# Performance work log

Measured on AMD Instinct MI355X. Metric: run time of the kernel, lower is better.

The kernel has to match this reference:

```python
import jax, jax.numpy as jnp
import numpy as np

B, T, D = 2, 2048, 2048
H, HD = 16, 128
I = 5632
CAP = 0.5
EPS = 1e-6
NEG = -1e9


def _rmsnorm(x, w):
    v = x.astype(jnp.float32)
    v = v * jax.lax.rsqrt(jnp.mean(v * v, axis=-1, keepdims=True) + EPS)
    return v.astype(x.dtype) * w


def _rotate_half(x):
    x1, x2 = jnp.split(x, 2, axis=-1)
    return jnp.concatenate([-x2, x1], axis=-1)


def setup_inputs() -> dict:
    key = jax.random.key(0)
    ks = jax.random.split(key, 20)
    s = 0.02
    inp = {
        'hidden_states': jax.random.normal(ks[0], (B, T, D), jnp.float32),
        'original': jax.random.normal(ks[1], (B, T, D), jnp.float32),
        'posterior': jax.random.normal(ks[2], (B, T, D), jnp.float32),
        'prior': jax.random.normal(ks[3], (B, T, D), jnp.float32),
        'cos': jax.random.normal(ks[4], (B, T, HD), jnp.float32),
        'sin': jax.random.normal(ks[5], (B, T, HD), jnp.float32),
        'position_ids': jax.random.randint(ks[6], (B, T), 0, T),
        'q_w': jax.random.normal(ks[7], (D, H * HD), jnp.float32) * s,
        'q_b': jnp.zeros((H * HD,), jnp.float32),
        'k_w': jax.random.normal(ks[8], (D, H * HD), jnp.float32) * s,
        'k_b': jnp.zeros((H * HD,), jnp.float32),
        'v_w': jax.random.normal(ks[9], (D, H * HD), jnp.float32) * s,
        'v_b': jnp.zeros((H * HD,), jnp.float32),
        'o_w': jax.random.normal(ks[10], (H * HD, D), jnp.float32) * s,
        'ln1_w': jnp.ones((D,), jnp.float32),
        'ln2_w': jnp.ones((D,), jnp.float32),
        'gate_w': jax.random.normal(ks[11], (D, I), jnp.float32) * s,
        'up_w': jax.random.normal(ks[12], (D, I), jnp.float32) * s,
        'down_w': jax.random.normal(ks[13], (I, D), jnp.float32) * s,
        'beta_ce': jnp.array(-0.5, jnp.float32),
        'beta_cu': jnp.array(-0.8, jnp.float32),
        'ce_off': jnp.array(1.0, jnp.float32),
    }
    return inp


def reference(hidden_states, original, posterior, prior, cos, sin, position_ids,
              q_w, q_b, k_w, k_b, v_w, v_b, o_w, ln1_w, ln2_w,
              gate_w, up_w, down_w, beta_ce, beta_cu, ce_off):
    Bt, Tt, Dt = hidden_states.shape
    K = int(CAP * Tt)  # tokens selected per batch row
    # --- router: surprise scores ---
    cu = jnp.linalg.norm(original - posterior, axis=-1)  # [B,T]
    ce = jnp.linalg.norm(posterior - prior, axis=-1)     # [B,T]
    scores = beta_cu * cu + beta_ce * (ce + ce_off)      # [B,T]
    # --- capacity top-k per batch row, keep temporal order ---
    _, topi = jax.lax.top_k(scores, K)                   # [B,K]
    token_idx2 = jnp.sort(topi, axis=-1)                 # [B,K]
    sel_scores = jnp.take_along_axis(scores, token_idx2, axis=1)  # [B,K]
    b_idx = jnp.repeat(jnp.arange(Bt), K)                # [S]
    t_idx = token_idx2.reshape(-1)                       # [S]
    S = Bt * K
    sel_h = hidden_states[b_idx, t_idx]                  # [S,D]
    cos_g = cos[b_idx, t_idx][None, None]                # [1,1,S,HD]
    sin_g = sin[b_idx, t_idx][None, None]
    # --- Qwen2 decoder block on the single gathered sequence [1,S,D] ---
    x = sel_h[None]
    h = _rmsnorm(x, ln1_w)
    q = (h @ q_w + q_b).reshape(1, S, H, HD).transpose(0, 2, 1, 3)  # [1,H,S,HD]
    k = (h @ k_w + k_b).reshape(1, S, H, HD).transpose(0, 2, 1, 3)
    v = (h @ v_w + v_b).reshape(1, S, H, HD).transpose(0, 2, 1, 3)
    q = q * cos_g + _rotate_half(q) * sin_g
    k = k * cos_g + _rotate_half(k) * sin_g
    att = jnp.einsum('bhqd,bhkd->bhqk', q, k) / np.sqrt(HD)
    causal = jnp.tril(jnp.ones((S, S), bool))
    att = jnp.where(causal, att, NEG)
    att = jax.nn.softmax(att.astype(jnp.float32), axis=-1).astype(x.dtype)
    o = jnp.einsum('bhqk,bhkd->bhqd', att, v)
    o = o.transpose(0, 2, 1, 3).reshape(1, S, H * HD) @ o_w
    x = x + o
    h = _rmsnorm(x, ln2_w)
    mlp = (jax.nn.silu(h @ gate_w) * (h @ up_w)) @ down_w
    x = x + mlp
    processed = x[0]                                     # [S,D]
    # --- gated update + scatter back ---
    gate = jax.nn.sigmoid(sel_scores.reshape(-1))[:, None]
    updated = sel_h + (processed - sel_h) * gate
    output = hidden_states.at[b_idx, t_idx].set(updated)
    return output
```

## Files before the change

### kernel.cpp

```cpp
#include <hip/hip_runtime.h>


typedef unsigned short u16;
typedef unsigned int u32;
typedef short bf16x8 __attribute__((ext_vector_type(8)));
typedef float f32x4 __attribute__((ext_vector_type(4)));

#define T_LEN 2048
#define D_DIM 2048
#define B_DIM 2
#define H_NUM 16
#define HD_DIM 128
#define I_DIM 5632
#define K_CAP 1024
#define S_TOT 2048
#define QKV_N 6144
#define GU_N 11264

__device__ __forceinline__ u16 f2bf(float f) {
  union { float f; u32 u; } a; a.f = f;
  u32 r = a.u + 0x7fffu + ((a.u >> 16) & 1u);
  return (u16)(r >> 16);
}
__device__ __forceinline__ float bf2f(u16 x) {
  return __uint_as_float((u32)x << 16);
}

__device__ __forceinline__ void gld_lds16(const void* g, void* l) {
  void* gg = const_cast<void*>(g);
  __builtin_amdgcn_global_load_lds(
      (__attribute__((address_space(1))) u32*)gg,
      (__attribute__((address_space(3))) u32*)l, 16, 0, 0);
}

__global__ __launch_bounds__(256)
void router_kernel(const float* __restrict__ orig, const float* __restrict__ post,
                   const float* __restrict__ prior, const float* __restrict__ bce,
                   const float* __restrict__ bcu, const float* __restrict__ coff,
                   float* __restrict__ scores) {
  const int row = blockIdx.x;
  const size_t base = (size_t)row * D_DIM;
  float s1 = 0.f, s2 = 0.f;
  for (int d = threadIdx.x * 4; d < D_DIM; d += 1024) {
    float4 o = *(const float4*)(orig + base + d);
    float4 p = *(const float4*)(post + base + d);
    float4 r = *(const float4*)(prior + base + d);
    float a;
    a = o.x - p.x; s1 += a * a;  a = o.y - p.y; s1 += a * a;
    a = o.z - p.z; s1 += a * a;  a = o.w - p.w; s1 += a * a;
    a = p.x - r.x; s2 += a * a;  a = p.y - r.y; s2 += a * a;
    a = p.z - r.z; s2 += a * a;  a = p.w - r.w; s2 += a * a;
  }
#pragma unroll
  for (int k = 32; k; k >>= 1) { s1 += __shfl_down(s1, k); s2 += __shfl_down(s2, k); }
  __shared__ float r1[4], r2[4];
  const int wv = threadIdx.x >> 6;
  if ((threadIdx.x & 63) == 0) { r1[wv] = s1; r2[wv] = s2; }
  __syncthreads();
  if (threadIdx.x == 0) {
    float cu = sqrtf(r1[0] + r1[1] + r1[2] + r1[3]);
    float ce = sqrtf(r2[0] + r2[1] + r2[2] + r2[3]);
    scores[row] = bcu[0] * cu + bce[0] * (ce + coff[0]);
  }
}

__global__ __launch_bounds__(256)
void rank_kernel(const float* __restrict__ scores, int* __restrict__ rnk) {
  const int b = blockIdx.y;
  const int t = blockIdx.x * 256 + threadIdx.x;
  __shared__ float s[T_LEN];
  for (int u = threadIdx.x; u < T_LEN; u += 256) s[u] = scores[b * T_LEN + u];
  __syncthreads();
  const float st = s[t];
  int r = 0;
  for (int u = 0; u < T_LEN; ++u) {
    float su = s[u];
    r += ((su > st) || (su == st && u < t)) ? 1 : 0;
  }
  rnk[b * T_LEN + t] = r;
}

__global__ __launch_bounds__(256)
void compact_kernel(const float* __restrict__ scores, const int* __restrict__ rnk,
                    int* __restrict__ tidx, float* __restrict__ gate) {
  const int b = blockIdx.x;
  const int base = b * T_LEN;
  __shared__ int csum[256];
  int f[8]; int loc = 0;
  const int t0 = threadIdx.x * 8;
#pragma unroll
  for (int i = 0; i < 8; ++i) { f[i] = (rnk[base + t0 + i] < K_CAP) ? 1 : 0; loc += f[i]; }
  csum[threadIdx.x] = loc;
  __syncthreads();
  if (threadIdx.x == 0) {
    int run = 0;
    for (int i = 0; i < 256; ++i) { int tmp = csum[i]; csum[i] = run; run += tmp; }
  }
  __syncthreads();
  int pos = csum[threadIdx.x];
#pragma unroll
  for (int i = 0; i < 8; ++i) {
    if (f[i]) {
      float sc = scores[base + t0 + i];
      tidx[b * K_CAP + pos] = t0 + i;
      gate[b * K_CAP + pos] = 1.f / (1.f + __expf(-sc));
      ++pos;
    }
  }
}

__global__ __launch_bounds__(256)
void transpose_bf16_kernel(const float* __restrict__ W, u16* __restrict__ Wt,
                           int K, int N) {
  __shared__ float tile[32][33];
  const int bn = blockIdx.x * 32, bk = blockIdx.y * 32;
  const int tx = threadIdx.x & 31, ty = threadIdx.x >> 5;
#pragma unroll
  for (int i = 0; i < 32; i += 8)
    tile[ty + i][tx] = W[(size_t)(bk + ty + i) * N + bn + tx];
  __syncthreads();
#pragma unroll
  for (int i = 0; i < 32; i += 8)
    Wt[(size_t)(bn + ty + i) * K + bk + tx] = f2bf(tile[tx][ty + i]);
}

__global__ __launch_bounds__(256)
void vtrans_kernel(const u16* __restrict__ qkv, u16* __restrict__ VT) {
  __shared__ u16 tile[32][34];
  const int s0 = blockIdx.x * 32;
  const int c0 = blockIdx.y * 32;
  const int tx = threadIdx.x & 31, ty = threadIdx.x >> 5;
#pragma unroll
  for (int i = 0; i < 32; i += 8)
    tile[ty + i][tx] = qkv[(size_t)(s0 + ty + i) * QKV_N + 4096 + c0 + tx];
  __syncthreads();
#pragma unroll
  for (int i = 0; i < 32; i += 8)
    VT[(size_t)(c0 + ty + i) * S_TOT + s0 + tx] = tile[tx][ty + i];
}

__global__ __launch_bounds__(256)
void rmsnorm_kernel(const float* __restrict__ X, const int* __restrict__ tidx,
                    const float* __restrict__ w, float* __restrict__ xcopy,
                    u16* __restrict__ Y) {
  const int s = blockIdx.x;
  const float* row;
  if (tidx) {
    const int b = s >> 10;
    const int t = tidx[s];
    row = X + ((size_t)b * T_LEN + t) * D_DIM;
  } else {
    row = X + (size_t)s * D_DIM;
  }
  const int d0 = threadIdx.x * 4;
  float4 v0 = *(const float4*)(row + d0);
  float4 v1 = *(const float4*)(row + d0 + 1024);
  float ss = v0.x*v0.x + v0.y*v0.y + v0.z*v0.z + v0.w*v0.w
           + v1.x*v1.x + v1.y*v1.y + v1.z*v1.z + v1.w*v1.w;
#pragma unroll
  for (int k = 32; k; k >>= 1) ss += __shfl_down(ss, k);
  __shared__ float red[4];
  if ((threadIdx.x & 63) == 0) red[threadIdx.x >> 6] = ss;
  __syncthreads();
  const float tot = red[0] + red[1] + red[2] + red[3];
  const float rms = rsqrtf(tot * (1.0f / D_DIM) + 1e-6f);
  if (xcopy) {
    *(float4*)(xcopy + (size_t)s * D_DIM + d0) = v0;
    *(float4*)(xcopy + (size_t)s * D_DIM + d0 + 1024) = v1;
  }
  const float4 w0 = *(const float4*)(w + d0);
  const float4 w1 = *(const float4*)(w + d0 + 1024);
  u16* yp = Y + (size_t)s * D_DIM;
  u32 a0 = (u32)f2bf(v0.x * rms * w0.x) | ((u32)f2bf(v0.y * rms * w0.y) << 16);
  u32 a1 = (u32)f2bf(v0.z * rms * w0.z) | ((u32)f2bf(v0.w * rms * w0.w) << 16);
  *(uint2*)(yp + d0) = make_uint2(a0, a1);
  u32 b0 = (u32)f2bf(v1.x * rms * w1.x) | ((u32)f2bf(v1.y * rms * w1.y) << 16);
  u32 b1 = (u32)f2bf(v1.z * rms * w1.z) | ((u32)f2bf(v1.w * rms * w1.w) << 16);
  *(uint2*)(yp + d0 + 1024) = make_uint2(b0, b1);
}

__global__ __launch_bounds__(256)
void gemm_bf16_kernel(const u16* __restrict__ A, const u16* __restrict__ Bt,
                      float* __restrict__ C, u16* __restrict__ Cbf,
                      const float* __restrict__ bias,
                      const float* __restrict__ resid, int N, int K) {
  __shared__ u16 As[128 * 32];
  __shared__ u16 Bs[128 * 32];
  const int tid = threadIdx.x;
  const int w = tid >> 6, l = tid & 63;
  const int row0 = blockIdx.y * 128, col0 = blockIdx.x * 128;
  const int wr = (w >> 1) * 64, wc = (w & 1) * 64;
  const int am = l & 15, ak = (l >> 4) * 8;
  const int srow = l >> 2, scol = (l & 3) * 8;

  f32x4 acc[4][4] = {};

  const u16* Abase = A + (size_t)(row0 + srow) * K + scol;
  const u16* Bbase = Bt + (size_t)(col0 + srow) * K + scol;
  const int R0 = (w * 2) * 16, R1 = (w * 2 + 1) * 16;

  for (int k0 = 0; k0 < K; k0 += 32) {
    gld_lds16(Abase + (size_t)R0 * K + k0, &As[R0 * 32]);
    gld_lds16(Abase + (size_t)R1 * K + k0, &As[R1 * 32]);
    gld_lds16(Bbase + (size_t)R0 * K + k0, &Bs[R0 * 32]);
    gld_lds16(Bbase + (size_t)R1 * K + k0, &Bs[R1 * 32]);
    __syncthreads();
    bf16x8 af[4], bfr[4];
#pragma unroll
    for (int i = 0; i < 4; ++i) af[i] = *(const bf16x8*)&As[(wr + i * 16 + am) * 32 + ak];
#pragma unroll
    for (int j = 0; j < 4; ++j) bfr[j] = *(const bf16x8*)&Bs[(wc + j * 16 + am) * 32 + ak];
#pragma unroll
    for (int i = 0; i < 4; ++i)
#pragma unroll
      for (int j = 0; j < 4; ++j)
        acc[i][j] = __builtin_amdgcn_mfma_f32_16x16x32_bf16(af[i], bfr[j], acc[i][j], 0, 0, 0);
    __syncthreads();
  }

  const int rb = wr + (l >> 4) * 4;
  const int cb = wc + (l & 15);
#pragma unroll
  for (int i = 0; i < 4; ++i) {
#pragma unroll
    for (int j = 0; j < 4; ++j) {
      const int colg = col0 + cb + j * 16;
      const float bv = bias ? bias[colg] : 0.0f;
#pragma unroll
      for (int r = 0; r < 4; ++r) {
        const int rowg = row0 + rb + i * 16 + r;
        const size_t idx = (size_t)rowg * N + colg;
        float v = acc[i][j][r] + bv;
        if (resid) v += resid[idx];
        if (Cbf) Cbf[idx] = f2bf(v);
        else C[idx] = v;
      }
    }
  }
}

__global__ __launch_bounds__(256)
void gemm_bf16_splitk_kernel(const u16* __restrict__ A, const u16* __restrict__ Bt,
                             float* __restrict__ P, int N, int K, int kLen) {
  __shared__ u16 As[128 * 32];
  __shared__ u16 Bs[128 * 32];
  const int tid = threadIdx.x;
  const int w = tid >> 6, l = tid & 63;
  const int row0 = blockIdx.y * 128, col0 = blockIdx.x * 128;
  const int kbeg = blockIdx.z * kLen, kend = kbeg + kLen;
  float* Pz = P + (size_t)blockIdx.z * S_TOT * N;
  const int wr = (w >> 1) * 64, wc = (w & 1) * 64;
  const int am = l & 15, ak = (l >> 4) * 8;
  const int srow = l >> 2, scol = (l & 3) * 8;

  f32x4 acc[4][4] = {};

  const u16* Abase = A + (size_t)(row0 + srow) * K + scol;
  const u16* Bbase = Bt + (size_t)(col0 + srow) * K + scol;
  const int R0 = (w * 2) * 16, R1 = (w * 2 + 1) * 16;

  for (int k0 = kbeg; k0 < kend; k0 += 32) {
    gld_lds16(Abase + (size_t)R0 * K + k0, &As[R0 * 32]);
    gld_lds16(Abase + (size_t)R1 * K + k0, &As[R1 * 32]);
    gld_lds16(Bbase + (size_t)R0 * K + k0, &Bs[R0 * 32]);
    gld_lds16(Bbase + (size_t)R1 * K + k0, &Bs[R1 * 32]);
    __syncthreads();
    bf16x8 af[4], bfr[4];
#pragma unroll
    for (int i = 0; i < 4; ++i) af[i] = *(const bf16x8*)&As[(wr + i * 16 + am) * 32 + ak];
#pragma unroll
    for (int j = 0; j < 4; ++j) bfr[j] = *(const bf16x8*)&Bs[(wc + j * 16 + am) * 32 + ak];
#pragma unroll
    for (int i = 0; i < 4; ++i)
#pragma unroll
      for (int j = 0; j < 4; ++j)
        acc[i][j] = __builtin_amdgcn_mfma_f32_16x16x32_bf16(af[i], bfr[j], acc[i][j], 0, 0, 0);
    __syncthreads();
  }

  const int rb = wr + (l >> 4) * 4;
  const int cb = wc + (l & 15);
#pragma unroll
  for (int i = 0; i < 4; ++i)
#pragma unroll
    for (int j = 0; j < 4; ++j) {
      const int colg = col0 + cb + j * 16;
#pragma unroll
      for (int r = 0; r < 4; ++r) {
        const int rowg = row0 + rb + i * 16 + r;
        Pz[(size_t)rowg * N + colg] = acc[i][j][r];
      }
    }
}

__global__ __launch_bounds__(256)
void add3_kernel(float* __restrict__ acc, const float* __restrict__ p1,
                 const float* __restrict__ resid) {
  const size_t i = ((size_t)blockIdx.x * 256 + threadIdx.x) * 4;
  float4 a = *(const float4*)(acc + i);
  float4 b = *(const float4*)(p1 + i);
  float4 c = *(const float4*)(resid + i);
  a.x += b.x + c.x; a.y += b.y + c.y; a.z += b.z + c.z; a.w += b.w + c.w;
  *(float4*)(acc + i) = a;
}

__global__ __launch_bounds__(256)
void down_finish_kernel(const float* __restrict__ P, const float* __restrict__ x1,
                        const int* __restrict__ tidx, const float* __restrict__ gate,
                        const float* __restrict__ hs, float* __restrict__ out) {
  const int s = blockIdx.x;
  const int b = s >> 10;
  const int t = tidx[s];
  const float gg = gate[s];
  const size_t src = (size_t)s * D_DIM;
  const size_t dst = ((size_t)b * T_LEN + t) * D_DIM;
  const size_t plane = (size_t)S_TOT * D_DIM;
  for (int d = threadIdx.x * 4; d < D_DIM; d += 1024) {
    float4 p0 = *(const float4*)(P + src + d);
    float4 p1 = *(const float4*)(P + plane + src + d);
    float4 xr = *(const float4*)(x1 + src + d);
    float4 hv = *(const float4*)(hs + dst + d);
    float4 r;
    r.x = hv.x + (p0.x + p1.x + xr.x - hv.x) * gg;
    r.y = hv.y + (p0.y + p1.y + xr.y - hv.y) * gg;
    r.z = hv.z + (p0.z + p1.z + xr.z - hv.z) * gg;
    r.w = hv.w + (p0.w + p1.w + xr.w - hv.w) * gg;
    *(float4*)(out + dst + d) = r;
  }
}

__global__ __launch_bounds__(256)
void rope_kernel(u16* __restrict__ qkv, const float* __restrict__ cosb,
                 const float* __restrict__ sinb, const int* __restrict__ tidx) {
  const int idx = blockIdx.x * 256 + threadIdx.x;
  const int d = idx & 63;
  const int h = (idx >> 6) & 15;
  const int s = idx >> 10;
  const int b = s >> 10;
  const int t = tidx[s];
  const size_t base = (size_t)s * QKV_N + h * 128 + d;
  const size_t cb = ((size_t)b * T_LEN + t) * HD_DIM + d;
  const float c1 = cosb[cb], sn1 = sinb[cb];
  const float c2 = cosb[cb + 64], sn2 = sinb[cb + 64];
  float x1v, x2v;
  x1v = bf2f(qkv[base]); x2v = bf2f(qkv[base + 64]);
  qkv[base] = f2bf(x1v * c1 - x2v * sn1);
  qkv[base + 64] = f2bf(x2v * c2 + x1v * sn2);
  x1v = bf2f(qkv[base + 2048]); x2v = bf2f(qkv[base + 2048 + 64]);
  qkv[base + 2048] = f2bf(x1v * c1 - x2v * sn1);
  qkv[base + 2048 + 64] = f2bf(x2v * c2 + x1v * sn2);
}

__global__ __launch_bounds__(512, 4)
void attn_mfma_kernel(const u16* __restrict__ QKV, const u16* __restrict__ VT,
                      u16* __restrict__ Og) {
  const int h  = blockIdx.y;
  const int bx = blockIdx.x;
  const int qt = (h < 8) ? (31 - bx) : bx;
  const int q0 = qt * 64;
  const int tid = threadIdx.x;
  const int l  = tid & 63;
  const int w  = tid >> 6;
  const int g  = w >> 2;
  const int wq = w & 3;
  const int lm = l & 15, lk = l >> 4;

  __shared__ __align__(16) unsigned char smem[65536];
  u16* Ks = (u16*)(smem + g * 16384);
  u16* Vt = (u16*)(smem + 32768 + g * 16384);
  u16* Ps = (u16*)(smem + g * 16384);

  const u16* Qg  = QKV + h * 128;
  const u16* Kg  = QKV + 2048 + h * 128;
  const u16* Vgt = VT + (size_t)h * 128 * S_TOT;

  bf16x8 qf[4];
  {
    const u16* qrow = Qg + (size_t)(q0 + wq * 16 + lm) * QKV_N;
#pragma unroll
    for (int ks = 0; ks < 4; ++ks) qf[ks] = *(const bf16x8*)&qrow[ks * 32 + lk * 8];
  }

  int ksrc[4], vsrc[4];
#pragma unroll
  for (int p = 0; p < 4; ++p) {
    const int ci = (wq * 4 + p) * 64 + l;
    const int kr = ci >> 4, kc = ci & 15;
    ksrc[p] = kr * QKV_N + ((kc ^ (kr & 7)) * 8);
    const int vr = ci >> 3, vc = ci & 7;
    vsrc[p] = vr * S_TOT + ((vc ^ (vr & 7)) * 8);
  }

  f32x4 oacc[8];
#pragma unroll
  for (int n = 0; n < 8; ++n) oacc[n] = (f32x4){0.f, 0.f, 0.f, 0.f};
  float m_run[4] = {-1e30f, -1e30f, -1e30f, -1e30f};
  float l_run[4] = {0.f, 0.f, 0.f, 0.f};

  const int ntiles = (g == 0) ? (qt / 2 + 1) : ((qt + 1) / 2);
  const int nmax = qt / 2 + 1;
  const float scale = 0.08838834764831845f;

  for (int it = 0; it < nmax; ++it) {
    const int kt = g + 2 * it;
    const int kv0 = kt * 64;
    const bool active = (it < ntiles);
    __syncthreads();
    if (active) {
#pragma unroll
      for (int p = 0; p < 4; ++p) {
        gld_lds16(Kg + (size_t)kv0 * QKV_N + ksrc[p], &Ks[(wq * 4 + p) * 512]);
        gld_lds16(Vgt + kv0 + vsrc[p],               &Vt[(wq * 4 + p) * 512]);
      }
    }
    __syncthreads();

    f32x4 sacc[4];
    if (active) {
#pragma unroll
      for (int j = 0; j < 4; ++j) sacc[j] = (f32x4){0.f, 0.f, 0.f, 0.f};
#pragma unroll
      for (int j = 0; j < 4; ++j) {
        const int row = j * 16 + lm;
#pragma unroll
        for (int ks = 0; ks < 4; ++ks) {
          const int c = ks * 4 + lk;
          const bf16x8 kf = *(const bf16x8*)&(
              (const unsigned char*)Ks)[row * 256 + ((c ^ (row & 7)) << 4)];
          sacc[j] = __builtin_amdgcn_mfma_f32_16x16x32_bf16(qf[ks], kf, sacc[j], 0, 0, 0);
        }
      }
    }
    __syncthreads();

    if (active) {
      float mx[4] = {-1e30f, -1e30f, -1e30f, -1e30f};
#pragma unroll
      for (int j = 0; j < 4; ++j) {
        const int colg = kv0 + j * 16 + lm;
#pragma unroll
        for (int r = 0; r < 4; ++r) {
          const int rowg = q0 + wq * 16 + lk * 4 + r;
          float s = sacc[j][r] * scale;
          s = (colg > rowg) ? -1e30f : s;
          sacc[j][r] = s;
          mx[r] = fmaxf(mx[r], s);
        }
      }
#pragma unroll
      for (int r = 0; r < 4; ++r)
#pragma unroll
        for (int dlt = 1; dlt < 16; dlt <<= 1)
          mx[r] = fmaxf(mx[r], __shfl_xor(mx[r], dlt));
      float alpha[4];
#pragma unroll
      for (int r = 0; r < 4; ++r) {
        const float mnew = fmaxf(m_run[r], mx[r]);
        const float al = __expf(m_run[r] - mnew);
        float sum = 0.f;
#pragma unroll
        for (int j = 0; j < 4; ++j) {
          const float pe = __expf(sacc[j][r] - mnew);
          sacc[j][r] = pe;
          sum += pe;
        }
#pragma unroll
        for (int dlt = 1; dlt < 16; dlt <<= 1) sum += __shfl_xor(sum, dlt);
        l_run[r] = l_run[r] * al + sum;
        m_run[r] = mnew;
        alpha[r] = al;
      }
#pragma unroll
      for (int n = 0; n < 8; ++n)
#pragma unroll
        for (int r = 0; r < 4; ++r) oacc[n][r] *= alpha[r];

#pragma unroll
      for (int j = 0; j < 4; ++j)
#pragma unroll
        for (int r = 0; r < 4; ++r) {
          const int row = wq * 16 + lk * 4 + r;
          *(u16*)&((unsigned char*)Ps)[row * 128 +
              (((j * 16 + lm) * 2) ^ ((row & 7) << 4))] = f2bf(sacc[j][r]);
        }

#pragma unroll
      for (int ks2 = 0; ks2 < 2; ++ks2) {
        const int prow = wq * 16 + lm;
        const bf16x8 pf = *(const bf16x8*)&(
            (const unsigned char*)Ps)[prow * 128 +
                ((ks2 * 64 + lk * 16) ^ ((prow & 7) << 4))];
#pragma unroll
        for (int n = 0; n < 8; ++n) {
          const int vrow = n * 16 + lm;
          const int vc = ks2 * 4 + lk;
          const bf16x8 vf = *(const bf16x8*)&(
              (const unsigned char*)Vt)[vrow * 128 + ((vc ^ (vrow & 7)) << 4)];
          oacc[n] = __builtin_amdgcn_mfma_f32_16x16x32_bf16(pf, vf, oacc[n], 0, 0, 0);
        }
      }
    }
  }

  __syncthreads();
  float* Obuf = (float*)smem;
  float* Mbuf = (float*)(smem + 33792);
  float* Lbuf = (float*)(smem + 34048);
  if (g == 1) {
#pragma unroll
    for (int r = 0; r < 4; ++r) {
      const int row = wq * 16 + lk * 4 + r;
      if (lm == 0) { Mbuf[row] = m_run[r]; Lbuf[row] = l_run[r]; }
#pragma unroll
      for (int n = 0; n < 8; ++n) Obuf[row * 132 + n * 16 + lm] = oacc[n][r];
    }
  }
  __syncthreads();
  if (g == 0) {
    float a0[4], a1[4], linv[4];
#pragma unroll
    for (int r = 0; r < 4; ++r) {
      const int row = wq * 16 + lk * 4 + r;
      const float m1 = Mbuf[row], l1 = Lbuf[row];
      const float M = fmaxf(m_run[r], m1);
      a0[r] = __expf(m_run[r] - M);
      a1[r] = __expf(m1 - M);
      linv[r] = 1.f / (a0[r] * l_run[r] + a1[r] * l1);
    }
#pragma unroll
    for (int n = 0; n < 8; ++n)
#pragma unroll
      for (int r = 0; r < 4; ++r) {
        const int row = wq * 16 + lk * 4 + r;
        const float o = (oacc[n][r] * a0[r] +
                         Obuf[row * 132 + n * 16 + lm] * a1[r]) * linv[r];
        Og[(size_t)(q0 + row) * 2048 + h * 128 + n * 16 + lm] = f2bf(o);
      }
  }
}

__global__ __launch_bounds__(256)
void silu_mul_kernel(const u16* __restrict__ gu, u16* __restrict__ out) {
  const size_t i = (size_t)blockIdx.x * 256 + threadIdx.x;
  const int s = (int)(i / 1408);
  const int c = (int)(i - (size_t)s * 1408);
  const uint2 g4 = *(const uint2*)&gu[(size_t)s * GU_N + c * 4];
  const uint2 u4 = *(const uint2*)&gu[(size_t)s * GU_N + I_DIM + c * 4];
  float g[4], u[4];
  g[0] = __uint_as_float(g4.x << 16); g[1] = __uint_as_float(g4.x & 0xffff0000u);
  g[2] = __uint_as_float(g4.y << 16); g[3] = __uint_as_float(g4.y & 0xffff0000u);
  u[0] = __uint_as_float(u4.x << 16); u[1] = __uint_as_float(u4.x & 0xffff0000u);
  u[2] = __uint_as_float(u4.y << 16); u[3] = __uint_as_float(u4.y & 0xffff0000u);
  u16 r[4];
#pragma unroll
  for (int j = 0; j < 4; ++j) r[j] = f2bf(g[j] * u[j] / (1.f + __expf(-g[j])));
  u32 a0 = (u32)r[0] | ((u32)r[1] << 16);
  u32 a1 = (u32)r[2] | ((u32)r[3] << 16);
  *(uint2*)&out[(size_t)s * I_DIM + c * 4] = make_uint2(a0, a1);
}

extern "C" void kernel_launch(void* const* d_in, const int* in_sizes, int n_in,
                              void* d_out, int out_size, void* d_ws, size_t ws_size,
                              hipStream_t stream) {
  (void)in_sizes; (void)n_in; (void)out_size; (void)ws_size;
  const float* hs    = (const float*)d_in[0];
  const float* orig  = (const float*)d_in[1];
  const float* post  = (const float*)d_in[2];
  const float* prior = (const float*)d_in[3];
  const float* cosb  = (const float*)d_in[4];
  const float* sinb  = (const float*)d_in[5];
  const float* q_w = (const float*)d_in[7];
  const float* q_b = (const float*)d_in[8];
  const float* k_w = (const float*)d_in[9];
  const float* k_b = (const float*)d_in[10];
  const float* v_w = (const float*)d_in[11];
  const float* v_b = (const float*)d_in[12];
  const float* o_w = (const float*)d_in[13];
  const float* ln1 = (const float*)d_in[14];
  const float* ln2 = (const float*)d_in[15];
  const float* gate_w = (const float*)d_in[16];
  const float* up_w   = (const float*)d_in[17];
  const float* down_w = (const float*)d_in[18];
  const float* beta_ce = (const float*)d_in[19];
  const float* beta_cu = (const float*)d_in[20];
  const float* ce_off  = (const float*)d_in[21];
  float* out = (float*)d_out;

  char* wsp = (char*)d_ws;
  size_t off = 0;
  auto alloc = [&](size_t n) -> char* {
    char* r = wsp + off; off += (n + 255) & ~(size_t)255; return r;
  };
  const size_t SD4 = (size_t)S_TOT * D_DIM * 4;

  float* scores  = (float*)alloc((size_t)B_DIM * T_LEN * 4);
  int*   rnk     = (int*)  alloc((size_t)B_DIM * T_LEN * 4);
  int*   tidx    = (int*)  alloc((size_t)S_TOT * 4);
  float* gatebuf = (float*)alloc((size_t)S_TOT * 4);
  float* qkvbias = (float*)alloc((size_t)QKV_N * 4);
  u16* qkvwt = (u16*)alloc((size_t)QKV_N * 2048 * 2);
  u16* owt   = (u16*)alloc((size_t)2048 * 2048 * 2);
  u16* guwt  = (u16*)alloc((size_t)GU_N * 2048 * 2);
  u16* dwt   = (u16*)alloc((size_t)2048 * I_DIM * 2);
  char* rA = alloc(SD4);
  float* selh = (float*)rA;
  u16*   h2   = (u16*)rA;
  char* rB = alloc((size_t)S_TOT * I_DIM * 2);
  u16* h1     = (u16*)rB;
  u16* o_attn = (u16*)rB;
  u16* mlp_in = (u16*)rB;
  char* rC = alloc((size_t)S_TOT * GU_N * 2);
  u16* qkv_bf = (u16*)rC;
  u16* gu_bf  = (u16*)rC;
  float* dpart = (float*)rC;
  float* x1  = (float*)alloc(SD4);
  float* x1p = (float*)alloc(SD4);
  (void)x1p;
  u16* vT = (u16*)x1;

  hipMemcpyAsync(out, hs, (size_t)B_DIM * T_LEN * D_DIM * 4,
                 hipMemcpyDeviceToDevice, stream);
  hipMemcpyAsync(qkvbias, q_b, 2048 * 4, hipMemcpyDeviceToDevice, stream);
  hipMemcpyAsync(qkvbias + 2048, k_b, 2048 * 4, hipMemcpyDeviceToDevice, stream);
  hipMemcpyAsync(qkvbias + 4096, v_b, 2048 * 4, hipMemcpyDeviceToDevice, stream);

  router_kernel<<<dim3(B_DIM * T_LEN), 256, 0, stream>>>(orig, post, prior,
                                                         beta_ce, beta_cu, ce_off, scores);
  rank_kernel<<<dim3(8, B_DIM), 256, 0, stream>>>(scores, rnk);
  compact_kernel<<<dim3(B_DIM), 256, 0, stream>>>(scores, rnk, tidx, gatebuf);

  transpose_bf16_kernel<<<dim3(64, 64), 256, 0, stream>>>(q_w, qkvwt, 2048, 2048);
  transpose_bf16_kernel<<<dim3(64, 64), 256, 0, stream>>>(k_w, qkvwt + (size_t)2048 * 2048, 2048, 2048);
  transpose_bf16_kernel<<<dim3(64, 64), 256, 0, stream>>>(v_w, qkvwt + (size_t)4096 * 2048, 2048, 2048);
  transpose_bf16_kernel<<<dim3(64, 64), 256, 0, stream>>>(o_w, owt, 2048, 2048);
  transpose_bf16_kernel<<<dim3(176, 64), 256, 0, stream>>>(gate_w, guwt, 2048, I_DIM);
  transpose_bf16_kernel<<<dim3(176, 64), 256, 0, stream>>>(up_w, guwt + (size_t)I_DIM * 2048, 2048, I_DIM);
  transpose_bf16_kernel<<<dim3(64, 176), 256, 0, stream>>>(down_w, dwt, I_DIM, 2048);

  rmsnorm_kernel<<<dim3(S_TOT), 256, 0, stream>>>(hs, tidx, ln1, selh, h1);

  gemm_bf16_kernel<<<dim3(48, 16), 256, 0, stream>>>(h1, qkvwt, nullptr, qkv_bf,
                                                     qkvbias, nullptr, QKV_N, 2048);
  rope_kernel<<<dim3((S_TOT * H_NUM * 64) / 256), 256, 0, stream>>>(qkv_bf, cosb, sinb, tidx);

  vtrans_kernel<<<dim3(64, 64), 256, 0, stream>>>(qkv_bf, vT);

  attn_mfma_kernel<<<dim3(32, H_NUM), 512, 0, stream>>>(qkv_bf, vT, o_attn);

  gemm_bf16_splitk_kernel<<<dim3(16, 16, 2), 256, 0, stream>>>(o_attn, owt, x1,
                                                               2048, 2048, 1024);
  add3_kernel<<<dim3((S_TOT * D_DIM) / 1024), 256, 0, stream>>>(
      x1, x1 + (size_t)S_TOT * D_DIM, selh);

  rmsnorm_kernel<<<dim3(S_TOT), 256, 0, stream>>>(x1, nullptr, ln2, nullptr, h2);

  gemm_bf16_kernel<<<dim3(88, 16), 256, 0, stream>>>(h2, guwt, nullptr, gu_bf,
                                                     nullptr, nullptr, GU_N, 2048);

  silu_mul_kernel<<<dim3((S_TOT * (I_DIM / 4)) / 256), 256, 0, stream>>>(gu_bf, mlp_in);

  gemm_bf16_splitk_kernel<<<dim3(16, 16, 2), 256, 0, stream>>>(mlp_in, dwt, dpart,
                                                               2048, 5632, 2816);

  down_finish_kernel<<<dim3(S_TOT), 256, 0, stream>>>(dpart, x1, tidx, gatebuf,
                                                      hs, out);
}
```

Measured before the change: 923.1 us.

## Add 256x256-tile 8-wave pipelined GEMM for QKV and gate/up projections

Introduces a new bf16 MFMA GEMM kernel with 256x256 output tiles, 512 threads, and direct global-to-LDS loads. It double-buffers LDS and interleaves A and B stage loads across two compute phases, using XOR-swizzled layouts, explicit waitcnt and barriers, and raised wave priority around the MFMA blocks. The kernel is used for the QKV and gate/up projections. It aims for more data reuse per tile and better overlap of memory with compute, at the cost of 64KB LDS per block and fewer blocks in the grid.

```diff
diff --git a/kernel.cpp b/kernel.cpp
--- a/kernel.cpp
+++ b/kernel.cpp
@@ -237,6 +237,107 @@
       }
     }
   }
+}
+
+__global__ __launch_bounds__(512, 2)
+void gemm_bf16_8ph_kernel(const u16* __restrict__ A, const u16* __restrict__ Bt,
+                          u16* __restrict__ Cbf, const float* __restrict__ bias,
+                          int N, int K) {
+  __shared__ __align__(16) unsigned char smem[65536];
+  const int tid = threadIdx.x;
+  const int l = tid & 63, w = tid >> 6;
+  const int wm = w >> 2, wn = w & 3;
+  const int lm = l & 15, lk = l >> 4;
+  const int row0 = blockIdx.y * 256, col0 = blockIdx.x * 256;
+  const int NT = K >> 5;
+
+  const int ci = w * 64 + l;
+  const int sr = ci >> 2;
+  const int sg = (ci & 3) ^ (sr & 3);
+  const u16* Ab = A + (size_t)row0 * K;
+  const u16* Bb = Bt + (size_t)col0 * K;
+
+  auto stage = [&](int buf, int mat, int half, int kt) {
+    const u16* src = mat ? Bb : Ab;
+    gld_lds16(src + (size_t)(half * 128 + sr) * K + kt * 32 + sg * 8,
+              smem + (buf << 15) + (mat << 14) + (half << 13) + (w << 10));
+  };
+
+  f32x4 acc[8][4] = {};
+
+  stage(0, 0, 0, 0); stage(0, 0, 1, 0); stage(0, 1, 0, 0); stage(0, 1, 1, 0);
+  stage(1, 1, 0, 1); stage(1, 1, 1, 1);
+  asm volatile("s_waitcnt vmcnt(2)" ::: "memory");
+  __builtin_amdgcn_s_barrier();
+
+  const int xo = ((lk << 4) ^ ((lm & 3) << 4));
+  for (int kt = 0; kt < NT; ++kt) {
+    const int buf = kt & 1;
+    const unsigned char* ab = smem + (buf << 15) + (wm << 13);
+    const unsigned char* bb = smem + (buf << 15) + 16384 + ((wn >> 1) << 13);
+    const int brow = (wn & 1) * 64;
+    bf16x8 afr[4], bfr[4];
+
+#pragma unroll
+    for (int j = 0; j < 4; ++j)
+      bfr[j] = *(const bf16x8*)(bb + (brow + j * 16 + lm) * 64 + xo);
+#pragma unroll
+    for (int i = 0; i < 4; ++i)
+      afr[i] = *(const bf16x8*)(ab + (i * 16 + lm) * 64 + xo);
+    if (kt + 1 < NT) {
+      stage(buf ^ 1, 0, 0, kt + 1);
+      stage(buf ^ 1, 0, 1, kt + 1);
+    }
+    __builtin_amdgcn_s_barrier();
+    asm volatile("s_waitcnt lgkmcnt(0)" ::: "memory");
+    __builtin_amdgcn_sched_barrier(0);
+    __builtin_amdgcn_s_setprio(1);
+#pragma unroll
+    for (int i = 0; i < 4; ++i)
+#pragma unroll
+      for (int j = 0; j < 4; ++j)
+        acc[i][j] = __builtin_amdgcn_mfma_f32_16x16x32_bf16(afr[i], bfr[j], acc[i][j], 0, 0, 0);
+    __builtin_amdgcn_s_setprio(0);
+    __builtin_amdgcn_s_barrier();
+
+#pragma unroll
+    for (int i = 0; i < 4; ++i)
+      afr[i] = *(const bf16x8*)(ab + ((i + 4) * 16 + lm) * 64 + xo);
+    if (kt + 2 < NT) {
+      stage(buf, 1, 0, kt + 2);
+      stage(buf, 1, 1, kt + 2);
+    }
+    __builtin_amdgcn_s_barrier();
+    asm volatile("s_waitcnt lgkmcnt(0)" ::: "memory");
+    __builtin_amdgcn_sched_barrier(0);
+    __builtin_amdgcn_s_setprio(1);
+#pragma unroll
+    for (int i = 0; i < 4; ++i)
+#pragma unroll
+      for (int j = 0; j < 4; ++j)
+        acc[i + 4][j] = __builtin_amdgcn_mfma_f32_16x16x32_bf16(afr[i], bfr[j], acc[i + 4][j], 0, 0, 0);
+    __builtin_amdgcn_s_setprio(0);
+    if (kt + 1 < NT) {
+      if (kt + 2 < NT) asm volatile("s_waitcnt vmcnt(2)" ::: "memory");
+      else             asm volatile("s_waitcnt vmcnt(0)" ::: "memory");
+    }
+    __builtin_amdgcn_s_barrier();
+  }
+
+  const int cb = col0 + wn * 64 + lm;
+  const int rb = row0 + wm * 128 + lk * 4;
+#pragma unroll
+  for (int i = 0; i < 8; ++i)
+#pragma unroll
+    for (int j = 0; j < 4; ++j) {
+      const int colg = cb + j * 16;
+      const float bv = bias ? bias[colg] : 0.0f;
+#pragma unroll
+      for (int r = 0; r < 4; ++r) {
+        const int rowg = rb + i * 16 + r;
+        Cbf[(size_t)rowg * N + colg] = f2bf(acc[i][j][r] + bv);
+      }
+    }
 }
 
 __global__ __launch_bounds__(256)
@@ -639,8 +740,8 @@
 
   rmsnorm_kernel<<<dim3(S_TOT), 256, 0, stream>>>(hs, tidx, ln1, selh, h1);
 
-  gemm_bf16_kernel<<<dim3(48, 16), 256, 0, stream>>>(h1, qkvwt, nullptr, qkv_bf,
-                                                     qkvbias, nullptr, QKV_N, 2048);
+  gemm_bf16_8ph_kernel<<<dim3(24, 8), 512, 0, stream>>>(h1, qkvwt, qkv_bf,
+                                                        qkvbias, QKV_N, 2048);
   rope_kernel<<<dim3((S_TOT * H_NUM * 64) / 256), 256, 0, stream>>>(qkv_bf, cosb, sinb, tidx);
 
   vtrans_kernel<<<dim3(64, 64), 256, 0, stream>>>(qkv_bf, vT);
@@ -654,8 +755,8 @@
 
   rmsnorm_kernel<<<dim3(S_TOT), 256, 0, stream>>>(x1, nullptr, ln2, nullptr, h2);
 
-  gemm_bf16_kernel<<<dim3(88, 16), 256, 0, stream>>>(h2, guwt, nullptr, gu_bf,
-                                                     nullptr, nullptr, GU_N, 2048);
+  gemm_bf16_8ph_kernel<<<dim3(44, 8), 512, 0, stream>>>(h2, guwt, gu_bf,
+                                                        nullptr, GU_N, 2048);
 
   silu_mul_kernel<<<dim3((S_TOT * (I_DIM / 4)) / 256), 256, 0, stream>>>(gu_bf, mlp_in);
 
```

New measurement: 921.2 us. About the same (-0.2%).
